# Optimization experiments

Measured on AMD Instinct MI355X. Metric: run time of the kernel, lower is better.

Reference implementation:

```python
import jax, jax.numpy as jnp
import numpy as np

N_NODES = 100000
N_EDGES = 1600000
IN_DIM = 256
OUT_DIM = 64


def setup_inputs() -> dict:
    key = jax.random.key(0)
    k1, k2, k3, k4, k5 = jax.random.split(key, 5)
    h = jax.random.normal(k1, (N_NODES, IN_DIM), dtype=jnp.float32)
    src = jax.random.randint(k2, (N_EDGES,), 0, N_NODES, dtype=jnp.int32)
    dst = jax.random.randint(k3, (N_EDGES,), 0, N_NODES, dtype=jnp.int32)
    # xavier_normal with gain for relu (sqrt(2))
    gain = float(np.sqrt(2.0))
    std_w = gain * float(np.sqrt(2.0 / (IN_DIM + OUT_DIM)))
    W = jax.random.normal(k4, (OUT_DIM, IN_DIM), dtype=jnp.float32) * std_w
    std_a = gain * float(np.sqrt(2.0 / (2 * OUT_DIM + 1)))
    a = jax.random.normal(k5, (2 * OUT_DIM,), dtype=jnp.float32) * std_a
    return {"h": h, "src": src, "dst": dst, "W": W, "a": a}


def reference(h, src, dst, W, a):
    # linear projection: W_h[n, out]
    W_h = h @ W.T
    # edge attention: e = relu(a . concat(W_h[src], W_h[dst]))
    a_src, a_dst = a[:OUT_DIM], a[OUT_DIM:]
    e = jax.nn.relu(W_h[src] @ a_src + W_h[dst] @ a_dst)  # [E]
    # segment softmax over incoming edges of each dst node
    m = jax.ops.segment_max(e, dst, num_segments=N_NODES)  # [N]
    ex = jnp.exp(e - m[dst])
    s = jax.ops.segment_sum(ex, dst, num_segments=N_NODES)  # [N]
    alpha = ex / s[dst]  # [E]
    # weighted scatter-sum of source messages
    h_N = jax.ops.segment_sum(alpha[:, None] * W_h[src], dst, num_segments=N_NODES)
    return h_N
```

## Files before the change

### kernel.cpp

```cpp
#include <hip/hip_runtime.h>
#include <hip/hip_bf16.h>
#include <math.h>
#include <stdint.h>

#define N_NODES 100000
#define N_EDGES 1600000
#define IN_DIM 256
#define OUT_DIM 64

#define CWIN  64
#define NCB   1563
#define NPART 256
#define EPP   (N_EDGES / NPART)
#define SCAN_N (NCB * NPART)
#define SCAN_BLK ((SCAN_N + 4095) / 4096)
#define MAXE  1536

#define GEMM_BLKS ((N_NODES + 255) / 256)


typedef __attribute__((ext_vector_type(8))) short bh8;
typedef __attribute__((ext_vector_type(4))) float f4;

typedef __attribute__((address_space(1))) const void GV;
typedef __attribute__((address_space(3))) void LV;

static __device__ __forceinline__ unsigned short f2bf(float f) {
    unsigned u = __float_as_uint(f);
    unsigned r = (u + 0x7FFFu + ((u >> 16) & 1u)) >> 16;
    return (unsigned short)r;
}

__global__ __launch_bounds__(64) void gat_wprep(const float* __restrict__ W,
                                                unsigned short* __restrict__ WB)
{
    const int cell = blockIdx.x * 64 + threadIdx.x;
    const int cl = cell & 15;
    const int nt = (cell >> 4) & 3;
    const int k16 = cell >> 6;
    const int col = nt * 16 + cl;
    const float4 lo = *(const float4*)(W + col * IN_DIM + k16 * 8);
    const float4 hi = *(const float4*)(W + col * IN_DIM + k16 * 8 + 4);
    unsigned short tmp[8];
    tmp[0] = f2bf(lo.x); tmp[1] = f2bf(lo.y);
    tmp[2] = f2bf(lo.z); tmp[3] = f2bf(lo.w);
    tmp[4] = f2bf(hi.x); tmp[5] = f2bf(hi.y);
    tmp[6] = f2bf(hi.z); tmp[7] = f2bf(hi.w);
    *(uint4*)&WB[(size_t)cell * 8] = *(uint4*)tmp;
}

__global__ __launch_bounds__(1024) void gat_gemm(
    const float* __restrict__ h, const unsigned short* __restrict__ WB,
    const float* __restrict__ a, unsigned short* __restrict__ WhB,
    float* __restrict__ p_src, float* __restrict__ p_dst,
    const int* __restrict__ dst, int* __restrict__ cur2dT)
{
    __shared__ __align__(16) unsigned short Wlds[64 * 256];

    const int t = threadIdx.x;

    if (blockIdx.x >= GEMM_BLKS) {
        const int part = blockIdx.x - GEMM_BLKS;
        int* lh = (int*)Wlds;
        for (int i = t; i < NCB; i += 1024) lh[i] = 0;
        __syncthreads();
        const int e0 = part * EPP;
        for (int e = e0 + t; e < e0 + EPP; e += 1024)
            atomicAdd(&lh[dst[e] >> 6], 1);
        __syncthreads();
        for (int i = t; i < NCB; i += 1024)
            cur2dT[part * NCB + i] = lh[i];
        return;
    }

    const int lane = t & 63;
    const int wv = t >> 6;
    const int cl = lane & 15;
    const int g  = lane >> 4;
    const int node0 = blockIdx.x * 256 + wv * 16;

    {
        #pragma unroll
        for (int i = 0; i < 2; ++i) {
            const int chunk = wv * 2 + i;
            __builtin_amdgcn_global_load_lds(
                (GV*)(WB + chunk * 512 + lane * 8),
                (LV*)(((char*)Wlds) + chunk * 1024), 16, 0, 0);
        }
    }
    __syncthreads();

    int row = node0 + cl;
    row = (row < N_NODES) ? row : N_NODES - 1;
    const float* __restrict__ hp = h + (size_t)row * IN_DIM + g * 8;

    f4 acc[4];
    #pragma unroll
    for (int nt = 0; nt < 4; ++nt) acc[nt] = (f4){0.f, 0.f, 0.f, 0.f};

    #pragma unroll
    for (int j = 0; j < 8; ++j) {
        const float4 lo = *(const float4*)(hp + j * 32);
        const float4 hi = *(const float4*)(hp + j * 32 + 4);
        bh8 af;
        af[0] = (short)f2bf(lo.x); af[1] = (short)f2bf(lo.y);
        af[2] = (short)f2bf(lo.z); af[3] = (short)f2bf(lo.w);
        af[4] = (short)f2bf(hi.x); af[5] = (short)f2bf(hi.y);
        af[6] = (short)f2bf(hi.z); af[7] = (short)f2bf(hi.w);

        #pragma unroll
        for (int nt = 0; nt < 4; ++nt) {
            const bh8 bf = *(const bh8*)&Wlds[(((j * 4 + g) * 64) + nt * 16 + cl) * 8];
            acc[nt] = __builtin_amdgcn_mfma_f32_16x16x32_bf16(af, bf, acc[nt], 0, 0, 0);
        }
    }

    float aS[4], aD[4];
    #pragma unroll
    for (int nt = 0; nt < 4; ++nt) {
        aS[nt] = a[nt * 16 + cl];
        aD[nt] = a[OUT_DIM + nt * 16 + cl];
    }

    #pragma unroll
    for (int r = 0; r < 4; ++r) {
        const int orow = node0 + g * 4 + r;
        float ps = 0.f, pd = 0.f;
        #pragma unroll
        for (int nt = 0; nt < 4; ++nt) {
            ps = fmaf(acc[nt][r], aS[nt], ps);
            pd = fmaf(acc[nt][r], aD[nt], pd);
        }
        #pragma unroll
        for (int o = 8; o > 0; o >>= 1) {
            ps += __shfl_xor(ps, o);
            pd += __shfl_xor(pd, o);
        }
        if (orow < N_NODES) {
            const unsigned lo2 = (unsigned)f2bf(acc[0][r]) |
                                 ((unsigned)f2bf(acc[1][r]) << 16);
            const unsigned hi2 = (unsigned)f2bf(acc[2][r]) |
                                 ((unsigned)f2bf(acc[3][r]) << 16);
            *(uint2*)&WhB[(size_t)orow * OUT_DIM + cl * 4] = make_uint2(lo2, hi2);
            if (cl == 0) { p_src[orow] = ps; p_dst[orow] = pd; }
        }
    }
}

__global__ __launch_bounds__(1024) void gat_scan1(int* __restrict__ data,
                                                  int* __restrict__ bsum)
{
    __shared__ int ts[1024];
    const int Lbase = blockIdx.x * 4096 + threadIdx.x * 4;
    int v[4], S[4];
    #pragma unroll
    for (int j = 0; j < 4; ++j) {
        const int L = Lbase + j;
        S[j] = (L & 255) * NCB + (L >> 8);
        v[j] = (L < SCAN_N) ? data[S[j]] : 0;
    }
    const int tsum = v[0] + v[1] + v[2] + v[3];
    ts[threadIdx.x] = tsum;
    __syncthreads();
    int val = tsum;
    for (int s = 1; s < 1024; s <<= 1) {
        const int add = (threadIdx.x >= s) ? ts[threadIdx.x - s] : 0;
        __syncthreads();
        val += add;
        ts[threadIdx.x] = val;
        __syncthreads();
    }
    int run = val - tsum;
    #pragma unroll
    for (int j = 0; j < 4; ++j) {
        const int L = Lbase + j;
        if (L < SCAN_N) data[S[j]] = run;
        run += v[j];
    }
    if (threadIdx.x == 1023) bsum[blockIdx.x] = val;
}

#define INLINE_BSUM_PREFIX(pbs, w0s)                                          \
{                                                                             \
    if (threadIdx.x < 128) {                                                  \
        const int v_ = (threadIdx.x < SCAN_BLK) ? bsum[threadIdx.x] : 0;      \
        int val_ = v_;                                                        \
        _Pragma("unroll")                                                     \
        for (int s_ = 1; s_ < 64; s_ <<= 1) {                                 \
            const int n_ = __shfl_up(val_, s_);                               \
            if ((threadIdx.x & 63) >= s_) val_ += n_;                         \
        }                                                                     \
        if (threadIdx.x == 63) w0s = val_;                                    \
        pbs[threadIdx.x] = val_ - v_;                                         \
    }                                                                         \
    __syncthreads();                                                          \
    if (threadIdx.x >= 64 && threadIdx.x < 128) pbs[threadIdx.x] += w0s;      \
    __syncthreads();                                                          \
}

__global__ __launch_bounds__(256) void gat_scatter_coarse(
    const int* __restrict__ src, const int* __restrict__ dst,
    const int* __restrict__ cur2dT, const int* __restrict__ bsum,
    int* __restrict__ ebufA)
{
    __shared__ int lcur[NCB];
    __shared__ int pbs[128];
    __shared__ int w0s;

    INLINE_BSUM_PREFIX(pbs, w0s)

    for (int i = threadIdx.x; i < NCB; i += 256) {
        const int L = i * NPART + blockIdx.x;
        lcur[i] = cur2dT[blockIdx.x * NCB + i] + pbs[L >> 12];
    }
    __syncthreads();
    const int e0 = blockIdx.x * EPP;
    for (int e = e0 + threadIdx.x; e < e0 + EPP; e += 256) {
        const int se = src[e], de = dst[e];
        const int pos = atomicAdd(&lcur[de >> 6], 1);
        ebufA[pos] = se | ((de & (CWIN - 1)) << 17);
    }
}

__global__ __launch_bounds__(256) void gat_agg_fused(
    const int* __restrict__ ebufA, const int* __restrict__ cur2dT,
    const int* __restrict__ bsum,
    const float* __restrict__ p_src, const float* __restrict__ p_dst,
    const unsigned short* __restrict__ Wh, float* __restrict__ out)
{
    __shared__ int2 ledge[MAXE];
    __shared__ int lhist[CWIN], lbase[CWIN];
    __shared__ float pdl[CWIN];
    __shared__ int pbs[128];
    __shared__ int w0s;

    const int t = threadIdx.x;
    const int cb = blockIdx.x;

    INLINE_BSUM_PREFIX(pbs, w0s)

    const int a0 = cur2dT[cb] + pbs[cb >> 4];
    int a1 = N_EDGES;
    if (cb < NCB - 1) a1 = cur2dT[cb + 1] + pbs[(cb + 1) >> 4];
    const int cnt = min(a1 - a0, MAXE);
    const int wbase = cb * CWIN;

    if (t < CWIN) {
        lhist[t] = 0;
        const int node = wbase + t;
        pdl[t] = (node < N_NODES) ? p_dst[node] : 0.f;
    }
    __syncthreads();

    int   ev[6], rk[6];
    float ps[6];
    #pragma unroll
    for (int j = 0; j < 6; ++j) {
        const int i = t + j * 256;
        ev[j] = 0; rk[j] = 0; ps[j] = 0.f;
        if (i < cnt) {
            const int e = ebufA[a0 + i];
            ev[j] = e;
            ps[j] = p_src[e & 0x1FFFF];
            rk[j] = atomicAdd(&lhist[(e >> 17) & (CWIN - 1)], 1);
        }
    }
    __syncthreads();

    if (t < 64) {
        const int own = lhist[t];
        int val = own;
        #pragma unroll
        for (int s = 1; s < 64; s <<= 1) {
            const int n = __shfl_up(val, s);
            if (t >= s) val += n;
        }
        lbase[t] = val - own;
    }
    __syncthreads();

    #pragma unroll
    for (int j = 0; j < 6; ++j) {
        const int i = t + j * 256;
        if (i < cnt) {
            const int e = ev[j];
            const int ln = (e >> 17) & (CWIN - 1);
            const float ex = __expf(fmaxf(ps[j] + pdl[ln], 0.f));
            ledge[lbase[ln] + rk[j]] = make_int2(e & 0x1FFFF, __float_as_int(ex));
        }
    }
    __syncthreads();

    const int lane = t & 63;
    const int wv = t >> 6;
    const int grp = lane >> 4;
    const int ci = lane & 15;
    const int c4 = ci * 4;

    #pragma unroll
    for (int rr = 0; rr < 4; ++rr) {
        const int ln = wv * 16 + rr * 4 + grp;
        const int node = wbase + ln;
        const int sb = lbase[ln];
        const int d  = (node < N_NODES) ? lhist[ln] : 0;

        float ssum = 0.f;
        float a0f = 0.f, a1f = 0.f, a2f = 0.f, a3f = 0.f;

        #pragma unroll 4
        for (int k = 0; k < d; ++k) {
            const int2 ed = ledge[sb + k];
            const float ex = __int_as_float(ed.y);
            const uint2 wr = *(const uint2*)(Wh + (size_t)ed.x * OUT_DIM + c4);
            ssum += ex;
            a0f = fmaf(ex, __uint_as_float(wr.x << 16), a0f);
            a1f = fmaf(ex, __uint_as_float(wr.x & 0xFFFF0000u), a1f);
            a2f = fmaf(ex, __uint_as_float(wr.y << 16), a2f);
            a3f = fmaf(ex, __uint_as_float(wr.y & 0xFFFF0000u), a3f);
        }

        if (node < N_NODES) {
            const float inv = (d > 0) ? 1.f / ssum : 0.f;
            float* ob = out + (size_t)node * OUT_DIM;
            ob[ci]      = a0f * inv;
            ob[16 + ci] = a1f * inv;
            ob[32 + ci] = a2f * inv;
            ob[48 + ci] = a3f * inv;
        }
    }
}

extern "C" void kernel_launch(void* const* d_in, const int* in_sizes, int n_in,
                              void* d_out, int out_size, void* d_ws, size_t ws_size,
                              hipStream_t stream)
{
    const float* h  = (const float*)d_in[0];
    const int* src  = (const int*)d_in[1];
    const int* dst  = (const int*)d_in[2];
    const float* W  = (const float*)d_in[3];
    const float* a  = (const float*)d_in[4];
    float* out = (float*)d_out;

    char* ws = (char*)d_ws;
    unsigned short* WhB = (unsigned short*)(ws);
    float* p_src   = (float*)(ws + 12800000);
    float* p_dst   = (float*)(ws + 13200000);
    int*   cur2dT  = (int*)  (ws + 13600000);
    int*   bsum    = (int*)  (ws + 15200512);
    int*   ebufA   = (int*)  (ws + 15200904);
    unsigned short* WB = (unsigned short*)(ws + 21601024);

    gat_wprep<<<32, 64, 0, stream>>>(W, WB);
    gat_gemm<<<GEMM_BLKS + NPART, 1024, 0, stream>>>(h, WB, a, WhB, p_src, p_dst,
                                                     dst, cur2dT);
    gat_scan1<<<SCAN_BLK, 1024, 0, stream>>>(cur2dT, bsum);
    gat_scatter_coarse<<<NPART, 256, 0, stream>>>(src, dst, cur2dT, bsum, ebufA);
    gat_agg_fused<<<NCB, 256, 0, stream>>>(ebufA, cur2dT, bsum, p_src, p_dst,
                                           WhB, out);
}
```

Baseline: 100.5 us.

## Regroup kernels: fuse histogram with W prep, GEMM with coarse scatter

Reorganizes the launch schedule so the edge histogram runs alongside W bf16 conversion in one kernel, and the dense projection GEMM runs in the same launch as the coarse edge scatter. This removes one kernel launch and lets the memory-heavy GEMM overlap with the atomic-heavy scatter, instead of overlapping the GEMM with the histogram. The scatter blocks now use 1024 threads and reuse the GEMM's LDS buffer for cursors, which keeps LDS usage at 32KB per block and may limit occupancy for the scatter part.

```diff
diff --git a/kernel.cpp b/kernel.cpp
--- a/kernel.cpp
+++ b/kernel.cpp
@@ -31,120 +31,38 @@
     return (unsigned short)r;
 }
 
-__global__ __launch_bounds__(64) void gat_wprep(const float* __restrict__ W,
-                                                unsigned short* __restrict__ WB)
-{
-    const int cell = blockIdx.x * 64 + threadIdx.x;
-    const int cl = cell & 15;
-    const int nt = (cell >> 4) & 3;
-    const int k16 = cell >> 6;
-    const int col = nt * 16 + cl;
-    const float4 lo = *(const float4*)(W + col * IN_DIM + k16 * 8);
-    const float4 hi = *(const float4*)(W + col * IN_DIM + k16 * 8 + 4);
-    unsigned short tmp[8];
-    tmp[0] = f2bf(lo.x); tmp[1] = f2bf(lo.y);
-    tmp[2] = f2bf(lo.z); tmp[3] = f2bf(lo.w);
-    tmp[4] = f2bf(hi.x); tmp[5] = f2bf(hi.y);
-    tmp[6] = f2bf(hi.z); tmp[7] = f2bf(hi.w);
-    *(uint4*)&WB[(size_t)cell * 8] = *(uint4*)tmp;
-}
-
-__global__ __launch_bounds__(1024) void gat_gemm(
-    const float* __restrict__ h, const unsigned short* __restrict__ WB,
-    const float* __restrict__ a, unsigned short* __restrict__ WhB,
-    float* __restrict__ p_src, float* __restrict__ p_dst,
-    const int* __restrict__ dst, int* __restrict__ cur2dT)
-{
-    __shared__ __align__(16) unsigned short Wlds[64 * 256];
-
+__global__ __launch_bounds__(1024) void gat_hist_wprep(
+    const int* __restrict__ dst, int* __restrict__ cur2dT,
+    const float* __restrict__ W, unsigned short* __restrict__ WB)
+{
     const int t = threadIdx.x;
 
-    if (blockIdx.x >= GEMM_BLKS) {
-        const int part = blockIdx.x - GEMM_BLKS;
-        int* lh = (int*)Wlds;
-        for (int i = t; i < NCB; i += 1024) lh[i] = 0;
-        __syncthreads();
-        const int e0 = part * EPP;
-        for (int e = e0 + t; e < e0 + EPP; e += 1024)
-            atomicAdd(&lh[dst[e] >> 6], 1);
-        __syncthreads();
-        for (int i = t; i < NCB; i += 1024)
-            cur2dT[part * NCB + i] = lh[i];
+    if (blockIdx.x >= NPART) {
+        const int cell = (blockIdx.x - NPART) * 1024 + t;
+        const int cl = cell & 15;
+        const int nt = (cell >> 4) & 3;
+        const int k16 = cell >> 6;
+        const int col = nt * 16 + cl;
+        const float4 lo = *(const float4*)(W + col * IN_DIM + k16 * 8);
+        const float4 hi = *(const float4*)(W + col * IN_DIM + k16 * 8 + 4);
+        unsigned short tmp[8];
+        tmp[0] = f2bf(lo.x); tmp[1] = f2bf(lo.y);
+        tmp[2] = f2bf(lo.z); tmp[3] = f2bf(lo.w);
+        tmp[4] = f2bf(hi.x); tmp[5] = f2bf(hi.y);
+        tmp[6] = f2bf(hi.z); tmp[7] = f2bf(hi.w);
+        *(uint4*)&WB[(size_t)cell * 8] = *(uint4*)tmp;
         return;
     }
 
-    const int lane = t & 63;
-    const int wv = t >> 6;
-    const int cl = lane & 15;
-    const int g  = lane >> 4;
-    const int node0 = blockIdx.x * 256 + wv * 16;
-
-    {
-        #pragma unroll
-        for (int i = 0; i < 2; ++i) {
-            const int chunk = wv * 2 + i;
-            __builtin_amdgcn_global_load_lds(
-                (GV*)(WB + chunk * 512 + lane * 8),
-                (LV*)(((char*)Wlds) + chunk * 1024), 16, 0, 0);
-        }
-    }
-    __syncthreads();
-
-    int row = node0 + cl;
-    row = (row < N_NODES) ? row : N_NODES - 1;
-    const float* __restrict__ hp = h + (size_t)row * IN_DIM + g * 8;
-
-    f4 acc[4];
-    #pragma unroll
-    for (int nt = 0; nt < 4; ++nt) acc[nt] = (f4){0.f, 0.f, 0.f, 0.f};
-
-    #pragma unroll
-    for (int j = 0; j < 8; ++j) {
-        const float4 lo = *(const float4*)(hp + j * 32);
-        const float4 hi = *(const float4*)(hp + j * 32 + 4);
-        bh8 af;
-        af[0] = (short)f2bf(lo.x); af[1] = (short)f2bf(lo.y);
-        af[2] = (short)f2bf(lo.z); af[3] = (short)f2bf(lo.w);
-        af[4] = (short)f2bf(hi.x); af[5] = (short)f2bf(hi.y);
-        af[6] = (short)f2bf(hi.z); af[7] = (short)f2bf(hi.w);
-
-        #pragma unroll
-        for (int nt = 0; nt < 4; ++nt) {
-            const bh8 bf = *(const bh8*)&Wlds[(((j * 4 + g) * 64) + nt * 16 + cl) * 8];
-            acc[nt] = __builtin_amdgcn_mfma_f32_16x16x32_bf16(af, bf, acc[nt], 0, 0, 0);
-        }
-    }
-
-    float aS[4], aD[4];
-    #pragma unroll
-    for (int nt = 0; nt < 4; ++nt) {
-        aS[nt] = a[nt * 16 + cl];
-        aD[nt] = a[OUT_DIM + nt * 16 + cl];
-    }
-
-    #pragma unroll
-    for (int r = 0; r < 4; ++r) {
-        const int orow = node0 + g * 4 + r;
-        float ps = 0.f, pd = 0.f;
-        #pragma unroll
-        for (int nt = 0; nt < 4; ++nt) {
-            ps = fmaf(acc[nt][r], aS[nt], ps);
-            pd = fmaf(acc[nt][r], aD[nt], pd);
-        }
-        #pragma unroll
-        for (int o = 8; o > 0; o >>= 1) {
-            ps += __shfl_xor(ps, o);
-            pd += __shfl_xor(pd, o);
-        }
-        if (orow < N_NODES) {
-            const unsigned lo2 = (unsigned)f2bf(acc[0][r]) |
-                                 ((unsigned)f2bf(acc[1][r]) << 16);
-            const unsigned hi2 = (unsigned)f2bf(acc[2][r]) |
-                                 ((unsigned)f2bf(acc[3][r]) << 16);
-            *(uint2*)&WhB[(size_t)orow * OUT_DIM + cl * 4] = make_uint2(lo2, hi2);
-            if (cl == 0) { p_src[orow] = ps; p_dst[orow] = pd; }
-        }
-    }
+    __shared__ int lh[NCB];
+    for (int i = t; i < NCB; i += 1024) lh[i] = 0;
+    __syncthreads();
+    const int e0 = blockIdx.x * EPP;
+    for (int e = e0 + t; e < e0 + EPP; e += 1024)
+        atomicAdd(&lh[dst[e] >> 6], 1);
+    __syncthreads();
+    for (int i = t; i < NCB; i += 1024)
+        cur2dT[blockIdx.x * NCB + i] = lh[i];
 }
 
 __global__ __launch_bounds__(1024) void gat_scan1(int* __restrict__ data,
@@ -198,27 +116,111 @@
     __syncthreads();                                                          \
 }
 
-__global__ __launch_bounds__(256) void gat_scatter_coarse(
+__global__ __launch_bounds__(1024) void gat_gemm_scatter(
+    const float* __restrict__ h, const unsigned short* __restrict__ WB,
+    const float* __restrict__ a, unsigned short* __restrict__ WhB,
+    float* __restrict__ p_src, float* __restrict__ p_dst,
     const int* __restrict__ src, const int* __restrict__ dst,
     const int* __restrict__ cur2dT, const int* __restrict__ bsum,
     int* __restrict__ ebufA)
 {
-    __shared__ int lcur[NCB];
+    __shared__ __align__(16) unsigned short Wlds[64 * 256];
     __shared__ int pbs[128];
     __shared__ int w0s;
 
-    INLINE_BSUM_PREFIX(pbs, w0s)
-
-    for (int i = threadIdx.x; i < NCB; i += 256) {
-        const int L = i * NPART + blockIdx.x;
-        lcur[i] = cur2dT[blockIdx.x * NCB + i] + pbs[L >> 12];
-    }
-    __syncthreads();
-    const int e0 = blockIdx.x * EPP;
-    for (int e = e0 + threadIdx.x; e < e0 + EPP; e += 256) {
-        const int se = src[e], de = dst[e];
-        const int pos = atomicAdd(&lcur[de >> 6], 1);
-        ebufA[pos] = se | ((de & (CWIN - 1)) << 17);
+    const int t = threadIdx.x;
+
+    if (blockIdx.x >= GEMM_BLKS) {
+        const int part = blockIdx.x - GEMM_BLKS;
+        int* lcur = (int*)Wlds;
+
+        INLINE_BSUM_PREFIX(pbs, w0s)
+
+        for (int i = t; i < NCB; i += 1024) {
+            const int L = i * NPART + part;
+            lcur[i] = cur2dT[part * NCB + i] + pbs[L >> 12];
+        }
+        __syncthreads();
+        const int e0 = part * EPP;
+        for (int e = e0 + t; e < e0 + EPP; e += 1024) {
+            const int se = src[e], de = dst[e];
+            const int pos = atomicAdd(&lcur[de >> 6], 1);
+            ebufA[pos] = se | ((de & (CWIN - 1)) << 17);
+        }
+        return;
+    }
+
+    const int lane = t & 63;
+    const int wv = t >> 6;
+    const int cl = lane & 15;
+    const int g  = lane >> 4;
+    const int node0 = blockIdx.x * 256 + wv * 16;
+
+    {
+        #pragma unroll
+        for (int i = 0; i < 2; ++i) {
+            const int chunk = wv * 2 + i;
+            __builtin_amdgcn_global_load_lds(
+                (GV*)(WB + chunk * 512 + lane * 8),
+                (LV*)(((char*)Wlds) + chunk * 1024), 16, 0, 0);
+        }
+    }
+    __syncthreads();
+
+    int row = node0 + cl;
+    row = (row < N_NODES) ? row : N_NODES - 1;
+    const float* __restrict__ hp = h + (size_t)row * IN_DIM + g * 8;
+
+    f4 acc[4];
+    #pragma unroll
+    for (int nt = 0; nt < 4; ++nt) acc[nt] = (f4){0.f, 0.f, 0.f, 0.f};
+
+    #pragma unroll
+    for (int j = 0; j < 8; ++j) {
+        const float4 lo = *(const float4*)(hp + j * 32);
+        const float4 hi = *(const float4*)(hp + j * 32 + 4);
+        bh8 af;
+        af[0] = (short)f2bf(lo.x); af[1] = (short)f2bf(lo.y);
+        af[2] = (short)f2bf(lo.z); af[3] = (short)f2bf(lo.w);
+        af[4] = (short)f2bf(hi.x); af[5] = (short)f2bf(hi.y);
+        af[6] = (short)f2bf(hi.z); af[7] = (short)f2bf(hi.w);
+
+        #pragma unroll
+        for (int nt = 0; nt < 4; ++nt) {
+            const bh8 bf = *(const bh8*)&Wlds[(((j * 4 + g) * 64) + nt * 16 + cl) * 8];
+            acc[nt] = __builtin_amdgcn_mfma_f32_16x16x32_bf16(af, bf, acc[nt], 0, 0, 0);
+        }
+    }
+
+    float aS[4], aD[4];
+    #pragma unroll
+    for (int nt = 0; nt < 4; ++nt) {
+        aS[nt] = a[nt * 16 + cl];
+        aD[nt] = a[OUT_DIM + nt * 16 + cl];
+    }
+
+    #pragma unroll
+    for (int r = 0; r < 4; ++r) {
+        const int orow = node0 + g * 4 + r;
+        float ps = 0.f, pd = 0.f;
+        #pragma unroll
+        for (int nt = 0; nt < 4; ++nt) {
+            ps = fmaf(acc[nt][r], aS[nt], ps);
+            pd = fmaf(acc[nt][r], aD[nt], pd);
+        }
+        #pragma unroll
+        for (int o = 8; o > 0; o >>= 1) {
+            ps += __shfl_xor(ps, o);
+            pd += __shfl_xor(pd, o);
+        }
+        if (orow < N_NODES) {
+            const unsigned lo2 = (unsigned)f2bf(acc[0][r]) |
+                                 ((unsigned)f2bf(acc[1][r]) << 16);
+            const unsigned hi2 = (unsigned)f2bf(acc[2][r]) |
+                                 ((unsigned)f2bf(acc[3][r]) << 16);
+            *(uint2*)&WhB[(size_t)orow * OUT_DIM + cl * 4] = make_uint2(lo2, hi2);
+            if (cl == 0) { p_src[orow] = ps; p_dst[orow] = pd; }
+        }
     }
 }
 
@@ -350,11 +352,10 @@
     int*   ebufA   = (int*)  (ws + 15200904);
     unsigned short* WB = (unsigned short*)(ws + 21601024);
 
-    gat_wprep<<<32, 64, 0, stream>>>(W, WB);
-    gat_gemm<<<GEMM_BLKS + NPART, 1024, 0, stream>>>(h, WB, a, WhB, p_src, p_dst,
-                                                     dst, cur2dT);
+    gat_hist_wprep<<<NPART + 2, 1024, 0, stream>>>(dst, cur2dT, W, WB);
     gat_scan1<<<SCAN_BLK, 1024, 0, stream>>>(cur2dT, bsum);
-    gat_scatter_coarse<<<NPART, 256, 0, stream>>>(src, dst, cur2dT, bsum, ebufA);
+    gat_gemm_scatter<<<GEMM_BLKS + NPART, 1024, 0, stream>>>(
+        h, WB, a, WhB, p_src, p_dst, src, dst, cur2dT, bsum, ebufA);
     gat_agg_fused<<<NCB, 256, 0, stream>>>(ebufA, cur2dT, bsum, p_src, p_dst,
                                            WhB, out);
 }
```

New measurement: 89.85 us. 10.6% less time.
